# Kernel optimization log

Hardware: AMD Instinct MI355X
Metric: run time of the kernel (lower is better)

## Reference

```python
import jax, jax.numpy as jnp
import numpy as np

TEMP = 0.1
ALPHA = 0.5
REG_W = 0.1
DTW_BETA = 0.1
DTW_SCALE = 10.0

BS, D, NF, NC = 128, 768, 64, 32


def _l2norm(x, eps=1e-12):
    return x / jnp.maximum(jnp.linalg.norm(x, axis=-1, keepdims=True), eps)


def _ce_diag(logits):
    # cross-entropy with targets = arange(n): positives on the diagonal
    lsm = jax.nn.log_softmax(logits, axis=-1)
    return -jnp.mean(jnp.diagonal(lsm))


def clip_info_ce(v, t, temp=TEMP):
    # CLIP-style symmetric InfoNCE on L2-normalized embeddings
    v = _l2norm(v)
    t = _l2norm(t)
    logits = (v @ t.T) / temp
    return 0.5 * (_ce_diag(logits) + _ce_diag(logits.T))


def ntxent(v, t, temp=TEMP, alpha=ALPHA):
    # SimCLR-style NT-Xent over the 2N concatenated views, alpha-weighted per direction
    n = v.shape[0]
    z = _l2norm(jnp.concatenate([v, t], axis=0))  # [2n, d]
    sim = (z @ z.T) / temp
    sim = jnp.where(jnp.eye(2 * n, dtype=bool), -1e9, sim)  # mask self-similarity
    lsm = jax.nn.log_softmax(sim, axis=-1)
    pos_idx = jnp.concatenate([jnp.arange(n) + n, jnp.arange(n)])
    pos = lsm[jnp.arange(2 * n), pos_idx]
    return alpha * (-jnp.mean(pos[:n])) + (1.0 - alpha) * (-jnp.mean(pos[n:]))


def _softmin3(a, b, c, beta):
    x = jnp.stack([a, b, c], axis=0)
    return -beta * jax.nn.logsumexp(-x / beta, axis=0)


def soft_dtw(cost, beta):
    # cost: [P, N, M] -> soft-DTW distance [P] via anti-causal DP (scan rows, scan cols)
    row0 = jnp.cumsum(cost[:, 0, :], axis=-1)  # [P, M], only-right path on first row

    def row_step(R_prev, cost_row):  # R_prev, cost_row: [P, M]
        r_first = cost_row[:, 0] + R_prev[:, 0]  # only-up move at j=0

        def col_step(r_left, inp):
            c, up, diag = inp  # each [P]
            r = c + _softmin3(r_left, up, diag, beta)
            return r, r

        xs = (cost_row[:, 1:].T, R_prev[:, 1:].T, R_prev[:, :-1].T)  # [M-1, P]
        _, rest = jax.lax.scan(col_step, r_first, xs)
        R_row = jnp.concatenate([r_first[None, :], rest], axis=0).T  # [P, M]
        return R_row, None

    R_last, _ = jax.lax.scan(row_step, row0, jnp.swapaxes(cost[:, 1:, :], 0, 1))
    return R_last[:, -1]


def dtw_contrastive_loss(embs_v, embs_t, beta=DTW_BETA, scale=DTW_SCALE):
    # embs_v: [B, F, D] (normalized), embs_t: [B, C, D] (normalized)
    B, Fn, _ = embs_v.shape
    C = embs_t.shape[1]
    sim = jnp.einsum('bfd,gcd->bgfc', embs_v, embs_t)  # all-pairs frame/token sims
    cost = 1.0 - sim
    D_mat = soft_dtw(cost.reshape(B * B, Fn, C), beta).reshape(B, B)
    logits = -scale * D_mat  # smaller alignment cost -> larger logit
    return 0.5 * (_ce_diag(logits) + _ce_diag(logits.T))


def setup_inputs() -> dict:
    key = jax.random.key(0)
    k1, k2, k3, k4, k5 = jax.random.split(key, 5)
    return {
        'video_embd': jax.random.normal(k1, (BS, D), dtype=jnp.float32),
        'text_embd_sent': jax.random.normal(k2, (BS, D), dtype=jnp.float32),
        'text_embd_cand': jax.random.normal(k3, (BS, NC, D), dtype=jnp.float32),
        'video_embd_frame': jax.random.normal(k4, (BS, NF, D), dtype=jnp.float32),
        'pos_step': jax.random.randint(k5, (BS,), 0, NC, dtype=jnp.int64 if jax.config.jax_enable_x64 else jnp.int32),
    }


def reference(video_embd, text_embd_sent, text_embd_cand, video_embd_frame, pos_step):
    loss_1 = clip_info_ce(video_embd, text_embd_sent)
    loss_2 = ntxent(video_embd, text_embd_sent)
    aggregate_text = jnp.mean(text_embd_cand, axis=1)
    loss_3 = clip_info_ce(video_embd, aggregate_text)
    loss_4 = clip_info_ce(text_embd_sent, aggregate_text)
    embs_v = _l2norm(video_embd_frame)
    embs_t = _l2norm(text_embd_cand)
    loss_dtw = dtw_contrastive_loss(embs_v, embs_t)
    return (loss_1 + loss_2 + loss_3 + loss_4 + REG_W * loss_dtw) / 5.0
```

## Files before the change

kernel.cpp:

```cpp
#include <hip/hip_runtime.h>
#include <stdint.h>

typedef unsigned short ushort_t;
typedef __attribute__((ext_vector_type(4))) float f32x4;
typedef __attribute__((ext_vector_type(8))) short short8;
typedef __attribute__((ext_vector_type(4))) ushort_t us4;
typedef __attribute__((ext_vector_type(4))) int i32x4;
typedef __attribute__((ext_vector_type(8))) int i32x8;

#define LDS_AS __attribute__((address_space(3)))
#define GLB_AS __attribute__((address_space(1)))

__device__ __forceinline__ ushort_t f2bf(float f) {
    uint32_t u = __float_as_uint(f);
    u += 0x7FFFu + ((u >> 16) & 1u);
    return (ushort_t)(u >> 16);
}

__device__ __forceinline__ float bf2f(ushort_t u) {
    return __uint_as_float(((uint32_t)u) << 16);
}

__device__ __forceinline__ float dpp_shr1(float x) {
    return __int_as_float(__builtin_amdgcn_update_dpp(
        __float_as_int(1e30f), __float_as_int(x), 0x138, 0xF, 0xF, false));
}

__device__ __forceinline__ uint32_t pk_fp8(float4 x) {
    int u = __builtin_amdgcn_cvt_pk_fp8_f32(x.x, x.y, 0, false);
    u = __builtin_amdgcn_cvt_pk_fp8_f32(x.z, x.w, u, true);
    return (uint32_t)u;
}

__global__ __launch_bounds__(256) void k_prep_all(
    const float* __restrict__ frame, const float* __restrict__ cand,
    const float* __restrict__ video, const float* __restrict__ sent,
    uint8_t* __restrict__ A8, uint8_t* __restrict__ B8, ushort_t* __restrict__ Zbf,
    float* __restrict__ P)
{
    if (blockIdx.x == 0) {
        for (int i = threadIdx.x; i < 1152; i += 256) P[i] = 0.0f;
    }
    const int w = threadIdx.x >> 6, ln = threadIdx.x & 63;
    const int r = blockIdx.x * 4 + w;
    float4 x0, x1, x2;
    bool isfp8 = (r < 12288);
    uint8_t* dst8 = nullptr;
    ushort_t* dstz = nullptr;
    if (r < 8192) {
        const float4* s = (const float4*)(frame + (size_t)r * 768);
        x0 = s[ln]; x1 = s[ln + 64]; x2 = s[ln + 128];
        dst8 = A8 + (size_t)r * 768;
    } else if (r < 12288) {
        int q = r - 8192;
        const float4* s = (const float4*)(cand + (size_t)q * 768);
        x0 = s[ln]; x1 = s[ln + 64]; x2 = s[ln + 128];
        dst8 = B8 + (size_t)q * 768;
    } else if (r < 12416) {
        int q = r - 12288;
        const float4* s = (const float4*)(video + (size_t)q * 768);
        x0 = s[ln]; x1 = s[ln + 64]; x2 = s[ln + 128];
        dstz = Zbf + (size_t)q * 768;
    } else if (r < 12544) {
        int q = r - 12416;
        const float4* s = (const float4*)(sent + (size_t)q * 768);
        x0 = s[ln]; x1 = s[ln + 64]; x2 = s[ln + 128];
        dstz = Zbf + (size_t)(128 + q) * 768;
    } else {
        int b = r - 12544;
        x0 = x1 = x2 = make_float4(0.f, 0.f, 0.f, 0.f);
        for (int k = 0; k < 32; ++k) {
            const float4* s = (const float4*)(cand + (size_t)(b * 32 + k) * 768);
            float4 y0 = s[ln], y1 = s[ln + 64], y2 = s[ln + 128];
            x0.x += y0.x; x0.y += y0.y; x0.z += y0.z; x0.w += y0.w;
            x1.x += y1.x; x1.y += y1.y; x1.z += y1.z; x1.w += y1.w;
            x2.x += y2.x; x2.y += y2.y; x2.z += y2.z; x2.w += y2.w;
        }
        const float s32 = 1.0f / 32.0f;
        x0.x *= s32; x0.y *= s32; x0.z *= s32; x0.w *= s32;
        x1.x *= s32; x1.y *= s32; x1.z *= s32; x1.w *= s32;
        x2.x *= s32; x2.y *= s32; x2.z *= s32; x2.w *= s32;
        dstz = Zbf + (size_t)(256 + b) * 768;
    }
    float ss = x0.x*x0.x + x0.y*x0.y + x0.z*x0.z + x0.w*x0.w
             + x1.x*x1.x + x1.y*x1.y + x1.z*x1.z + x1.w*x1.w
             + x2.x*x2.x + x2.y*x2.y + x2.z*x2.z + x2.w*x2.w;
    #pragma unroll
    for (int off = 32; off > 0; off >>= 1) ss += __shfl_xor(ss, off);
    float sc = 1.0f / fmaxf(sqrtf(ss), 1e-12f);
    x0.x *= sc; x0.y *= sc; x0.z *= sc; x0.w *= sc;
    x1.x *= sc; x1.y *= sc; x1.z *= sc; x1.w *= sc;
    x2.x *= sc; x2.y *= sc; x2.z *= sc; x2.w *= sc;
    if (isfp8) {
        uint32_t* d32 = (uint32_t*)dst8;
        d32[ln] = pk_fp8(x0); d32[ln + 64] = pk_fp8(x1); d32[ln + 128] = pk_fp8(x2);
    } else {
        us4 u0, u1, u2;
        u0.x = f2bf(x0.x); u0.y = f2bf(x0.y); u0.z = f2bf(x0.z); u0.w = f2bf(x0.w);
        u1.x = f2bf(x1.x); u1.y = f2bf(x1.y); u1.z = f2bf(x1.z); u1.w = f2bf(x1.w);
        u2.x = f2bf(x2.x); u2.y = f2bf(x2.y); u2.z = f2bf(x2.z); u2.w = f2bf(x2.w);
        us4* d4 = (us4*)dstz;
        d4[ln] = u0; d4[ln + 64] = u1; d4[ln + 128] = u2;
    }
}

__global__ __launch_bounds__(256, 4) void k_fused(
    const uint8_t* __restrict__ A, const uint8_t* __restrict__ B,
    const ushort_t* __restrict__ Z,
    float* __restrict__ G, float* __restrict__ P, float* __restrict__ Dm)
{
    __shared__ __align__(16) ushort_t lds[16384];
    const int t = threadIdx.x;
    const int lane = t & 63, w = t >> 6;
    const int lr = lane & 15, lk = lane >> 4;

    if (blockIdx.x >= 2048) {
        ushort_t* As = lds;
        ushort_t* Bs = lds + 8192;
        const int bx = blockIdx.x - 2048;
        const int m0 = (bx / 3) * 128, n0 = (bx % 3) * 128;
        const int wr = w >> 1, wc = w & 1;
        f32x4 acc[4][4] = {};
        for (int k0 = 0; k0 < 768; k0 += 64) {
            #pragma unroll
            for (int ii = 0; ii < 4; ++ii) {
                int idx = ii * 256 + t;
                int row = idx >> 3, kc = (idx & 7) * 8;
                __builtin_amdgcn_global_load_lds(
                    (const GLB_AS void*)(Z + (size_t)(m0 + row) * 768 + (k0 + kc)),
                    (LDS_AS void*)(As + idx * 8), 16, 0, 0);
            }
            #pragma unroll
            for (int ii = 0; ii < 4; ++ii) {
                int idx = ii * 256 + t;
                int row = idx >> 3, kc = (idx & 7) * 8;
                __builtin_amdgcn_global_load_lds(
                    (const GLB_AS void*)(Z + (size_t)(n0 + row) * 768 + (k0 + kc)),
                    (LDS_AS void*)(Bs + idx * 8), 16, 0, 0);
            }
            __syncthreads();
            #pragma unroll
            for (int kk = 0; kk < 2; ++kk) {
                short8 av[4], bv[4];
                #pragma unroll
                for (int f = 0; f < 4; ++f)
                    av[f] = *(const short8*)(As + (wr * 64 + f * 16 + lr) * 64 + kk * 32 + lk * 8);
                #pragma unroll
                for (int f = 0; f < 4; ++f)
                    bv[f] = *(const short8*)(Bs + (wc * 64 + f * 16 + lr) * 64 + kk * 32 + lk * 8);
                #pragma unroll
                for (int fr = 0; fr < 4; ++fr)
                    #pragma unroll
                    for (int fc = 0; fc < 4; ++fc)
                        acc[fr][fc] = __builtin_amdgcn_mfma_f32_16x16x32_bf16(av[fr], bv[fc], acc[fr][fc], 0, 0, 0);
            }
            __syncthreads();
        }
        #pragma unroll
        for (int fr = 0; fr < 4; ++fr)
            #pragma unroll
            for (int fc = 0; fc < 4; ++fc) {
                int col = n0 + wc * 64 + fc * 16 + lr;
                #pragma unroll
                for (int q = 0; q < 4; ++q) {
                    int row = m0 + wr * 64 + fr * 16 + lk * 4 + q;
                    G[(size_t)row * 384 + col] = 10.0f * acc[fr][fc][q];
                }
            }
        #pragma unroll
        for (int fr = 0; fr < 4; ++fr)
            #pragma unroll
            for (int q = 0; q < 4; ++q) {
                float e = 0.0f;
                #pragma unroll
                for (int fc = 0; fc < 4; ++fc)
                    e += expf(10.0f * acc[fr][fc][q] - 10.0f);
                #pragma unroll
                for (int off = 1; off < 16; off <<= 1) e += __shfl_xor(e, off);
                if (lr == 0) {
                    int row = m0 + wr * 64 + fr * 16 + lk * 4 + q;
                    atomicAdd(&P[row * 3 + (bx % 3)], e);
                }
            }
        return;
    }

    uint8_t* lds8 = (uint8_t*)lds;
    const int wr = w >> 1, wc = w & 1;
    const int sw = lr & 7;
    const int lin = blockIdx.x;
    const int xcd = lin & 7, idx = lin >> 3;
    const int ntl = idx >> 3;
    const int mt  = xcd * 8 + (idx & 7);
    const int m0 = mt * 128, n0 = ntl * 128;

    f32x4 acc[4][4] = {};

    #pragma unroll 1
    for (int k0 = 0; k0 < 6; ++k0) {
        #pragma unroll
        for (int i = 0; i < 4; ++i) {
            int s = i * 256 + t, row = s >> 3, c16 = s & 7;
            int g = (c16 ^ (row & 7)) * 16;
            __builtin_amdgcn_global_load_lds(
                (const GLB_AS void*)(A + (size_t)(m0 + row) * 768 + k0 * 128 + g),
                (LDS_AS void*)(lds8 + s * 16), 16, 0, 0);
            __builtin_amdgcn_global_load_lds(
                (const GLB_AS void*)(B + (size_t)(n0 + row) * 768 + k0 * 128 + g),
                (LDS_AS void*)(lds8 + 16384 + s * 16), 16, 0, 0);
        }
        __syncthreads();
        i32x8 av[4];
        #pragma unroll
        for (int f = 0; f < 4; ++f) {
            const uint8_t* rb = lds8 + (wr * 64 + f * 16 + lr) * 128;
            i32x4 lo = *(const i32x4*)(rb + (((lk * 2) ^ sw) * 16));
            i32x4 hi = *(const i32x4*)(rb + (((lk * 2 + 1) ^ sw) * 16));
            av[f][0] = lo[0]; av[f][1] = lo[1]; av[f][2] = lo[2]; av[f][3] = lo[3];
            av[f][4] = hi[0]; av[f][5] = hi[1]; av[f][6] = hi[2]; av[f][7] = hi[3];
        }
        #pragma unroll
        for (int fc = 0; fc < 4; ++fc) {
            const uint8_t* rb = lds8 + 16384 + (wc * 64 + fc * 16 + lr) * 128;
            i32x4 lo = *(const i32x4*)(rb + (((lk * 2) ^ sw) * 16));
            i32x4 hi = *(const i32x4*)(rb + (((lk * 2 + 1) ^ sw) * 16));
            i32x8 bv;
            bv[0] = lo[0]; bv[1] = lo[1]; bv[2] = lo[2]; bv[3] = lo[3];
            bv[4] = hi[0]; bv[5] = hi[1]; bv[6] = hi[2]; bv[7] = hi[3];
            #pragma unroll
            for (int fr = 0; fr < 4; ++fr)
                acc[fr][fc] = __builtin_amdgcn_mfma_scale_f32_16x16x128_f8f6f4(
                    av[fr], bv, acc[fr][fc], 0, 0,
                    0, 0x7F7F7F7F, 0, 0x7F7F7F7F);
        }
        __syncthreads();
    }

    ushort_t* qd = lds + w * 4096;
    #pragma unroll
    for (int fr = 0; fr < 4; ++fr)
        #pragma unroll
        for (int fc = 0; fc < 4; ++fc)
            #pragma unroll
            for (int q = 0; q < 4; ++q)
                qd[(fr * 16 + lk * 4 + q) * 64 + fc * 16 + lr] = f2bf(acc[fr][fc][q]);

    const float K10 = 14.4269504088896340f;
    const float BIG = 1e30f;
    const int j = lane & 31, pr = lane >> 5;
    const bool isj0 = (j == 0);
    float rp = BIG, rp2 = BIG, dg0 = 0.0f;

    #pragma unroll 5
    for (int s = 0; s < 95; ++s) {
        float up = dpp_shr1(rp);
        float dg = dpp_shr1(rp2);
        if (isj0) { up = BIG; dg = dg0; }
        int ii = s - j;
        int iic = ii < 0 ? 0 : (ii > 63 ? 63 : ii);
        float c = fmaf(bf2f(qd[iic * 64 + lane]), -K10, K10);
        float mn, md, mx;
        asm("v_min3_f32 %0, %1, %2, %3" : "=v"(mn) : "v"(rp), "v"(up), "v"(dg));
        asm("v_med3_f32 %0, %1, %2, %3" : "=v"(md) : "v"(rp), "v"(up), "v"(dg));
        asm("v_max3_f32 %0, %1, %2, %3" : "=v"(mx) : "v"(rp), "v"(up), "v"(dg));
        float e = __builtin_amdgcn_exp2f(mn - md) + __builtin_amdgcn_exp2f(mn - mx);
        float r = c + mn - __builtin_amdgcn_logf(1.0f + e);
        bool act = (unsigned)ii < 64u;
        rp2 = act ? rp : rp2;
        rp  = act ? r  : rp;
        dg0 = BIG;
    }
    if (j == 31) {
        int b  = mt * 2 + wr;
        int bp = ntl * 4 + wc * 2 + pr;
        Dm[(size_t)b * 128 + bp] = rp * (1.0f / K10);
    }
}

__global__ __launch_bounds__(256) void k_rowloss(
    const float* __restrict__ G, const float* __restrict__ P,
    const float* __restrict__ Dm, float* __restrict__ rowloss)
{
    const int w = threadIdx.x >> 6, ln = threadIdx.x & 63;
    const int i = blockIdx.x * 4 + w;
    float d1 = G[(size_t)i * 384 + 128 + i];
    float d3 = G[(size_t)i * 384 + 256 + i];
    float d4 = G[(size_t)(128 + i) * 384 + 256 + i];
    float l1 = 0.5f * ((10.0f + logf(P[i * 3 + 1]) - d1) + (10.0f + logf(P[(128 + i) * 3 + 0]) - d1));
    float l3 = 0.5f * ((10.0f + logf(P[i * 3 + 2]) - d3) + (10.0f + logf(P[(256 + i) * 3 + 0]) - d3));
    float l4 = 0.5f * ((10.0f + logf(P[(128 + i) * 3 + 2]) - d4) + (10.0f + logf(P[(256 + i) * 3 + 1]) - d4));
    float ntr = P[i * 3 + 0] + P[i * 3 + 1] - expf(G[(size_t)i * 384 + i] - 10.0f);
    float ntc = P[(128 + i) * 3 + 0] + P[(128 + i) * 3 + 1]
              - expf(G[(size_t)(128 + i) * 384 + 128 + i] - 10.0f);
    float nt = 0.5f * (10.0f + logf(ntr) - d1) + 0.5f * (10.0f + logf(ntc) - d1);
    float v0 = -10.0f * Dm[i * 128 + ln],        v1 = -10.0f * Dm[i * 128 + 64 + ln];
    float c0 = -10.0f * Dm[ln * 128 + i],        c1 = -10.0f * Dm[(64 + ln) * 128 + i];
    float mxr = fmaxf(v0, v1), mxc = fmaxf(c0, c1);
    #pragma unroll
    for (int off = 32; off > 0; off >>= 1) {
        mxr = fmaxf(mxr, __shfl_xor(mxr, off));
        mxc = fmaxf(mxc, __shfl_xor(mxc, off));
    }
    float sr = expf(v0 - mxr) + expf(v1 - mxr);
    float sc = expf(c0 - mxc) + expf(c1 - mxc);
    #pragma unroll
    for (int off = 32; off > 0; off >>= 1) {
        sr += __shfl_xor(sr, off);
        sc += __shfl_xor(sc, off);
    }
    float dd = -10.0f * Dm[i * 128 + i];
    float ld = 0.5f * ((mxr + logf(sr) - dd) + (mxc + logf(sc) - dd));
    if (ln == 0) rowloss[i] = l1 + l3 + l4 + nt + 0.1f * ld;
}

__global__ __launch_bounds__(128) void k_sum(const float* __restrict__ rowloss, float* __restrict__ out)
{
    int i = threadIdx.x;
    float tot = rowloss[i];
    #pragma unroll
    for (int o = 32; o > 0; o >>= 1) tot += __shfl_down(tot, o);
    __shared__ float sm[2];
    if ((i & 63) == 0) sm[i >> 6] = tot;
    __syncthreads();
    if (i == 0) out[0] = (sm[0] + sm[1]) / (128.0f * 5.0f);
}

extern "C" void kernel_launch(void* const* d_in, const int* in_sizes, int n_in,
                              void* d_out, int out_size, void* d_ws, size_t ws_size,
                              hipStream_t stream)
{
    (void)in_sizes; (void)n_in; (void)out_size; (void)ws_size;
    const float* video = (const float*)d_in[0];
    const float* sent  = (const float*)d_in[1];
    const float* cand  = (const float*)d_in[2];
    const float* frame = (const float*)d_in[3];

    char* ws = (char*)d_ws;
    size_t off = 0;
    auto alloc = [&](size_t b) { void* p = ws + off; off = (off + b + 255) & ~(size_t)255; return p; };
    uint8_t*  A8  = (uint8_t*)alloc((size_t)8192 * 768);
    uint8_t*  B8  = (uint8_t*)alloc((size_t)4096 * 768);
    ushort_t* Zbf = (ushort_t*)alloc((size_t)384 * 768 * 2);
    float*    G   = (float*)alloc((size_t)384 * 384 * 4);
    float*    P   = (float*)alloc((size_t)1152 * 4);
    float*    Dm  = (float*)alloc((size_t)128 * 128 * 4);
    float*    RL  = (float*)alloc((size_t)128 * 4);

    k_prep_all <<<3168, 256, 0, stream>>>(frame, cand, video, sent, A8, B8, Zbf, P);
    k_fused    <<<2057, 256, 0, stream>>>(A8, B8, Zbf, G, P, Dm);
    k_rowloss  <<<32, 256, 0, stream>>>(G, P, Dm, RL);
    k_sum      <<<1, 128, 0, stream>>>(RL, (float*)d_out);
}
```

Before: 90.08 us.

## Make DTW blocks persistent over four tiles, overlapping soft-DTW with next GEMM

Each DTW block now handles four consecutive N-tiles instead of one, cutting the grid from 2048 to 512 DTW blocks. The soft-DTW recurrence for the previous tile runs interleaved with the MFMA k-loop of the next tile, using a separate LDS region for the cost matrix, so the serial DP latency can hide behind GEMM loads and matrix ops. LDS doubles and occupancy hints drop from 4 to 2 blocks per CU. Less parallelism and fewer resident waves may reduce latency hiding.

```diff
diff --git a/kernel.cpp b/kernel.cpp
--- a/kernel.cpp
+++ b/kernel.cpp
@@ -104,20 +104,20 @@
     }
 }
 
-__global__ __launch_bounds__(256, 4) void k_fused(
+__global__ __launch_bounds__(256, 2) void k_fused(
     const uint8_t* __restrict__ A, const uint8_t* __restrict__ B,
     const ushort_t* __restrict__ Z,
     float* __restrict__ G, float* __restrict__ P, float* __restrict__ Dm)
 {
-    __shared__ __align__(16) ushort_t lds[16384];
+    __shared__ __align__(16) ushort_t lds[32768];
     const int t = threadIdx.x;
     const int lane = t & 63, w = t >> 6;
     const int lr = lane & 15, lk = lane >> 4;
 
-    if (blockIdx.x >= 2048) {
+    if (blockIdx.x >= 512) {
         ushort_t* As = lds;
         ushort_t* Bs = lds + 8192;
-        const int bx = blockIdx.x - 2048;
+        const int bx = blockIdx.x - 512;
         const int m0 = (bx / 3) * 128, n0 = (bx % 3) * 128;
         const int wr = w >> 1, wc = w & 1;
         f32x4 acc[4][4] = {};
@@ -186,95 +186,112 @@
     }
 
     uint8_t* lds8 = (uint8_t*)lds;
+    ushort_t* qd = lds + 16384 + w * 4096;
     const int wr = w >> 1, wc = w & 1;
     const int sw = lr & 7;
     const int lin = blockIdx.x;
     const int xcd = lin & 7, idx = lin >> 3;
-    const int ntl = idx >> 3;
     const int mt  = xcd * 8 + (idx & 7);
-    const int m0 = mt * 128, n0 = ntl * 128;
-
-    f32x4 acc[4][4] = {};
-
-    #pragma unroll 1
-    for (int k0 = 0; k0 < 6; ++k0) {
-        #pragma unroll
-        for (int i = 0; i < 4; ++i) {
-            int s = i * 256 + t, row = s >> 3, c16 = s & 7;
-            int g = (c16 ^ (row & 7)) * 16;
-            __builtin_amdgcn_global_load_lds(
-                (const GLB_AS void*)(A + (size_t)(m0 + row) * 768 + k0 * 128 + g),
-                (LDS_AS void*)(lds8 + s * 16), 16, 0, 0);
-            __builtin_amdgcn_global_load_lds(
-                (const GLB_AS void*)(B + (size_t)(n0 + row) * 768 + k0 * 128 + g),
-                (LDS_AS void*)(lds8 + 16384 + s * 16), 16, 0, 0);
-        }
-        __syncthreads();
-        i32x8 av[4];
-        #pragma unroll
-        for (int f = 0; f < 4; ++f) {
-            const uint8_t* rb = lds8 + (wr * 64 + f * 16 + lr) * 128;
-            i32x4 lo = *(const i32x4*)(rb + (((lk * 2) ^ sw) * 16));
-            i32x4 hi = *(const i32x4*)(rb + (((lk * 2 + 1) ^ sw) * 16));
-            av[f][0] = lo[0]; av[f][1] = lo[1]; av[f][2] = lo[2]; av[f][3] = lo[3];
-            av[f][4] = hi[0]; av[f][5] = hi[1]; av[f][6] = hi[2]; av[f][7] = hi[3];
-        }
-        #pragma unroll
-        for (int fc = 0; fc < 4; ++fc) {
-            const uint8_t* rb = lds8 + 16384 + (wc * 64 + fc * 16 + lr) * 128;
-            i32x4 lo = *(const i32x4*)(rb + (((lk * 2) ^ sw) * 16));
-            i32x4 hi = *(const i32x4*)(rb + (((lk * 2 + 1) ^ sw) * 16));
-            i32x8 bv;
-            bv[0] = lo[0]; bv[1] = lo[1]; bv[2] = lo[2]; bv[3] = lo[3];
-            bv[4] = hi[0]; bv[5] = hi[1]; bv[6] = hi[2]; bv[7] = hi[3];
-            #pragma unroll
-            for (int fr = 0; fr < 4; ++fr)
-                acc[fr][fc] = __builtin_amdgcn_mfma_scale_f32_16x16x128_f8f6f4(
-                    av[fr], bv, acc[fr][fc], 0, 0,
-                    0, 0x7F7F7F7F, 0, 0x7F7F7F7F);
-        }
-        __syncthreads();
-    }
-
-    ushort_t* qd = lds + w * 4096;
-    #pragma unroll
-    for (int fr = 0; fr < 4; ++fr)
-        #pragma unroll
-        for (int fc = 0; fc < 4; ++fc)
-            #pragma unroll
-            for (int q = 0; q < 4; ++q)
-                qd[(fr * 16 + lk * 4 + q) * 64 + fc * 16 + lr] = f2bf(acc[fr][fc][q]);
+    const int ng  = idx >> 3;
+    const int m0 = mt * 128;
 
     const float K10 = 14.4269504088896340f;
     const float BIG = 1e30f;
     const int j = lane & 31, pr = lane >> 5;
     const bool isj0 = (j == 0);
     float rp = BIG, rp2 = BIG, dg0 = 0.0f;
-
-    #pragma unroll 5
-    for (int s = 0; s < 95; ++s) {
-        float up = dpp_shr1(rp);
-        float dg = dpp_shr1(rp2);
-        if (isj0) { up = BIG; dg = dg0; }
-        int ii = s - j;
-        int iic = ii < 0 ? 0 : (ii > 63 ? 63 : ii);
-        float c = fmaf(bf2f(qd[iic * 64 + lane]), -K10, K10);
-        float mn, md, mx;
-        asm("v_min3_f32 %0, %1, %2, %3" : "=v"(mn) : "v"(rp), "v"(up), "v"(dg));
-        asm("v_med3_f32 %0, %1, %2, %3" : "=v"(md) : "v"(rp), "v"(up), "v"(dg));
-        asm("v_max3_f32 %0, %1, %2, %3" : "=v"(mx) : "v"(rp), "v"(up), "v"(dg));
-        float e = __builtin_amdgcn_exp2f(mn - md) + __builtin_amdgcn_exp2f(mn - mx);
-        float r = c + mn - __builtin_amdgcn_logf(1.0f + e);
-        bool act = (unsigned)ii < 64u;
-        rp2 = act ? rp : rp2;
-        rp  = act ? r  : rp;
-        dg0 = BIG;
-    }
-    if (j == 31) {
-        int b  = mt * 2 + wr;
-        int bp = ntl * 4 + wc * 2 + pr;
-        Dm[(size_t)b * 128 + bp] = rp * (1.0f / K10);
-    }
+    int pb = 0, pbp = 0;
+
+#define DTW_STEP(S) { \
+    float up = dpp_shr1(rp); \
+    float dg = dpp_shr1(rp2); \
+    if (isj0) { up = BIG; dg = dg0; } \
+    int ii = (S) - j; \
+    int iic = ii < 0 ? 0 : (ii > 63 ? 63 : ii); \
+    float c = fmaf(bf2f(qd[iic * 64 + lane]), -K10, K10); \
+    float mn, md, mx; \
+    asm("v_min3_f32 %0, %1, %2, %3" : "=v"(mn) : "v"(rp), "v"(up), "v"(dg)); \
+    asm("v_med3_f32 %0, %1, %2, %3" : "=v"(md) : "v"(rp), "v"(up), "v"(dg)); \
+    asm("v_max3_f32 %0, %1, %2, %3" : "=v"(mx) : "v"(rp), "v"(up), "v"(dg)); \
+    float e = __builtin_amdgcn_exp2f(mn - md) + __builtin_amdgcn_exp2f(mn - mx); \
+    float r = c + mn - __builtin_amdgcn_logf(1.0f + e); \
+    bool act = (unsigned)ii < 64u; \
+    rp2 = act ? rp : rp2; \
+    rp  = act ? r  : rp; \
+    dg0 = BIG; \
+}
+
+    #pragma unroll 1
+    for (int tt = 0; tt < 4; ++tt) {
+        const int ntl = ng * 4 + tt;
+        const int n0 = ntl * 128;
+        f32x4 acc[4][4] = {};
+
+        #pragma unroll 1
+        for (int k0 = 0; k0 < 6; ++k0) {
+            #pragma unroll
+            for (int i = 0; i < 4; ++i) {
+                int s = i * 256 + t, row = s >> 3, c16 = s & 7;
+                int g = (c16 ^ (row & 7)) * 16;
+                __builtin_amdgcn_global_load_lds(
+                    (const GLB_AS void*)(A + (size_t)(m0 + row) * 768 + k0 * 128 + g),
+                    (LDS_AS void*)(lds8 + s * 16), 16, 0, 0);
+                __builtin_amdgcn_global_load_lds(
+                    (const GLB_AS void*)(B + (size_t)(n0 + row) * 768 + k0 * 128 + g),
+                    (LDS_AS void*)(lds8 + 16384 + s * 16), 16, 0, 0);
+            }
+            __syncthreads();
+            i32x8 av[4];
+            #pragma unroll
+            for (int f = 0; f < 4; ++f) {
+                const uint8_t* rb = lds8 + (wr * 64 + f * 16 + lr) * 128;
+                i32x4 lo = *(const i32x4*)(rb + (((lk * 2) ^ sw) * 16));
+                i32x4 hi = *(const i32x4*)(rb + (((lk * 2 + 1) ^ sw) * 16));
+                av[f][0] = lo[0]; av[f][1] = lo[1]; av[f][2] = lo[2]; av[f][3] = lo[3];
+                av[f][4] = hi[0]; av[f][5] = hi[1]; av[f][6] = hi[2]; av[f][7] = hi[3];
+            }
+            #pragma unroll
+            for (int fc = 0; fc < 4; ++fc) {
+                const uint8_t* rb = lds8 + 16384 + (wc * 64 + fc * 16 + lr) * 128;
+                i32x4 lo = *(const i32x4*)(rb + (((lk * 2) ^ sw) * 16));
+                i32x4 hi = *(const i32x4*)(rb + (((lk * 2 + 1) ^ sw) * 16));
+                i32x8 bv;
+                bv[0] = lo[0]; bv[1] = lo[1]; bv[2] = lo[2]; bv[3] = lo[3];
+                bv[4] = hi[0]; bv[5] = hi[1]; bv[6] = hi[2]; bv[7] = hi[3];
+                #pragma unroll
+                for (int fr = 0; fr < 4; ++fr)
+                    acc[fr][fc] = __builtin_amdgcn_mfma_scale_f32_16x16x128_f8f6f4(
+                        av[fr], bv, acc[fr][fc], 0, 0,
+                        0, 0x7F7F7F7F, 0, 0x7F7F7F7F);
+            }
+            if (tt > 0) {
+                #pragma unroll
+                for (int q = 0; q < 16; ++q) DTW_STEP(k0 * 16 + q)
+            }
+            __syncthreads();
+        }
+
+        if (tt > 0 && j == 31)
+            Dm[(size_t)pb * 128 + pbp] = rp * (1.0f / K10);
+
+        #pragma unroll
+        for (int fr = 0; fr < 4; ++fr)
+            #pragma unroll
+            for (int fc = 0; fc < 4; ++fc)
+                #pragma unroll
+                for (int q = 0; q < 4; ++q)
+                    qd[(fr * 16 + lk * 4 + q) * 64 + fc * 16 + lr] = f2bf(acc[fr][fc][q]);
+
+        rp = BIG; rp2 = BIG; dg0 = 0.0f;
+        pb = mt * 2 + wr;
+        pbp = ntl * 4 + wc * 2 + pr;
+    }
+
+    #pragma unroll 4
+    for (int s = 0; s < 96; ++s) DTW_STEP(s)
+    if (j == 31)
+        Dm[(size_t)pb * 128 + pbp] = rp * (1.0f / K10);
+#undef DTW_STEP
 }
 
 __global__ __launch_bounds__(256) void k_rowloss(
@@ -347,7 +364,7 @@
     float*    RL  = (float*)alloc((size_t)128 * 4);
 
     k_prep_all <<<3168, 256, 0, stream>>>(frame, cand, video, sent, A8, B8, Zbf, P);
-    k_fused    <<<2057, 256, 0, stream>>>(A8, B8, Zbf, G, P, Dm);
+    k_fused    <<<521, 256, 0, stream>>>(A8, B8, Zbf, G, P, Dm);
     k_rowloss  <<<32, 256, 0, stream>>>(G, P, Dm, RL);
     k_sum      <<<1, 128, 0, stream>>>(RL, (float*)d_out);
 }
```

Result: slower. 98.05 us (+8.9%).
